# Kernel tuning notes

Hardware: AMD Instinct MI355X
Metric: run time of the kernel (lower is better)

The kernel has to match this reference:

```python
import jax, jax.numpy as jnp
import numpy as np

NUM_LEVELS = 16
FEATS_PER_LEVEL = 2
LOG2_HASHMAP = 19
TABLE_SIZE = 1 << LOG2_HASHMAP
BASE_RES = 16
DESIRED_RES = 4096
PER_LEVEL_SCALE = float(np.exp(np.log(DESIRED_RES / BASE_RES) / (NUM_LEVELS - 1)))
PRIMES = (np.uint32(1), np.uint32(2654435761), np.uint32(805459861))
N_POINTS = 2_000_000


def _level_features(x, table, level):
    # x: [N,3] in [0,1]; table: [TABLE_SIZE, F]
    scale = BASE_RES * (PER_LEVEL_SCALE ** level) - 1.0
    res = int(np.ceil(scale)) + 1
    dense = (res ** 3) <= TABLE_SIZE  # tcnn uses dense indexing when grid fits
    pos = x * scale + 0.5
    pos0 = jnp.floor(pos)
    w = pos - pos0                     # trilinear weights, [N,3]
    base = pos0.astype(jnp.uint32)
    out = jnp.zeros((x.shape[0], table.shape[1]), dtype=table.dtype)
    for c in range(8):                 # 8 corners of the voxel
        offs = [(c >> d) & 1 for d in range(3)]
        pc = [jnp.minimum(base[:, d] + np.uint32(offs[d]), np.uint32(res - 1)) for d in range(3)]
        if dense:
            idx = pc[0] + pc[1] * np.uint32(res) + pc[2] * np.uint32(res * res)
        else:
            idx = (pc[0] * PRIMES[0]) ^ (pc[1] * PRIMES[1]) ^ (pc[2] * PRIMES[2])
            idx = idx & np.uint32(TABLE_SIZE - 1)
        wt = jnp.ones(x.shape[0], dtype=x.dtype)
        for d in range(3):
            wt = wt * (w[:, d] if offs[d] else (1.0 - w[:, d]))
        out = out + wt[:, None] * table[idx.astype(jnp.int32)]
    return out


def hashgrid_encode(x, tables):
    # x: [N,3] in [0,1]; tables: [L, TABLE_SIZE, F] -> [N, L*F]
    return jnp.concatenate(
        [_level_features(x, tables[l], l) for l in range(NUM_LEVELS)], axis=-1)


def setup_inputs() -> dict:
    key = jax.random.key(0)
    k1, k2, k3, k4, k5 = jax.random.split(key, 5)
    points = jax.random.uniform(k1, (N_POINTS, 3), dtype=jnp.float32)
    # tcnn hashgrid init: uniform(-1e-4, 1e-4)
    tables = jax.random.uniform(k2, (NUM_LEVELS, TABLE_SIZE, FEATS_PER_LEVEL),
                                minval=-1e-4, maxval=1e-4, dtype=jnp.float32)
    def kaiming(k, fan_out, fan_in):
        bound = np.sqrt(2.0) * np.sqrt(3.0 / fan_in)
        return jax.random.uniform(k, (fan_out, fan_in), minval=-bound, maxval=bound,
                                  dtype=jnp.float32)
    W1 = kaiming(k3, 32, 32)
    W2 = kaiming(k4, 32, 32)
    W3 = kaiming(k5, 4, 32)
    aabb = jnp.stack([jnp.zeros(3, jnp.float32), jnp.ones(3, jnp.float32)])
    return {"points": points, "tables": tables, "W1": W1, "W2": W2, "W3": W3,
            "aabb": aabb}


def reference(points, tables, W1, W2, W3, aabb):
    texc = jnp.clip((points - aabb[0][None, :]) / (aabb[1] - aabb[0])[None, :], 0.0, 1.0)
    enc = hashgrid_encode(texc, tables)            # [N, 32]
    h = jax.nn.relu(enc @ W1.T)
    h = jax.nn.relu(h @ W2.T)
    out = h @ W3.T                                 # [N, 4]
    mn = jnp.array([0.0, 0.0, 0.0, 0.01], dtype=out.dtype)
    mx = jnp.array([1.0, 1.0, 1.0, 1.0], dtype=out.dtype)
    return jax.nn.sigmoid(out) * (mx - mn) + mn
```

## Files before the change

kernel.cpp:

```cpp
#include <hip/hip_runtime.h>
#include <cmath>


namespace {
constexpr int kLevels = 16;
constexpr unsigned kTableSize = 1u << 19;

typedef _Float16 half2_t __attribute__((ext_vector_type(2)));

struct LevelParams {
  float scale[kLevels];
  unsigned res[kLevels];
  int dense[kLevels];
};
}

__global__ __launch_bounds__(256)
void conv_tables_kernel(const float2* __restrict__ src, half2_t* __restrict__ dst,
                        int n_entries,
                        const float* __restrict__ W1, const float* __restrict__ W2,
                        const float* __restrict__ W3, half2_t* __restrict__ Wh)
{
  int i = blockIdx.x * blockDim.x + threadIdx.x;
  if (i < 512) {
    Wh[i] = half2_t{(_Float16)W1[2 * i], (_Float16)W1[2 * i + 1]};
  } else if (i < 1024) {
    int t = i - 512;
    Wh[512 + t] = half2_t{(_Float16)W2[2 * t], (_Float16)W2[2 * t + 1]};
  } else if (i < 1088) {
    int t = i - 1024;
    Wh[1024 + t] = half2_t{(_Float16)W3[2 * t], (_Float16)W3[2 * t + 1]};
  }
  int stride = gridDim.x * blockDim.x;
  for (; i < n_entries; i += stride) {
    float2 v = src[i];
    dst[i] = half2_t{(_Float16)v.x, (_Float16)v.y};
  }
}

__global__ __launch_bounds__(256)
void encode_kernel(const float* __restrict__ points,
                   const half2_t* __restrict__ tables,
                   const float* __restrict__ aabb,
                   half2_t* __restrict__ enc,
                   LevelParams lp, int n, int bpl)
{
  int l = blockIdx.x / bpl;
  int blk = blockIdx.x - l * bpl;
  int i0 = blk * 512 + threadIdx.x;
  int i1 = i0 + 256;
  if (i0 >= n) return;
  bool validB = (i1 < n);
  int i1c = validB ? i1 : i0;

  float a0x = aabb[0], a0y = aabb[1], a0z = aabb[2];
  float a1x = aabb[3], a1y = aabb[4], a1z = aabb[5];
  float s = lp.scale[l];
  unsigned res = lp.res[l];
  bool dense = (lp.dense[l] != 0);
  unsigned rm1 = res - 1u;
  unsigned res2 = res * res;
  const half2_t* tab = tables + (size_t)l * kTableSize;

  float xA = fminf(fmaxf((points[3 * i0 + 0] - a0x) / (a1x - a0x), 0.f), 1.f);
  float yA = fminf(fmaxf((points[3 * i0 + 1] - a0y) / (a1y - a0y), 0.f), 1.f);
  float zA = fminf(fmaxf((points[3 * i0 + 2] - a0z) / (a1z - a0z), 0.f), 1.f);
  float xB = fminf(fmaxf((points[3 * i1c + 0] - a0x) / (a1x - a0x), 0.f), 1.f);
  float yB = fminf(fmaxf((points[3 * i1c + 1] - a0y) / (a1y - a0y), 0.f), 1.f);
  float zB = fminf(fmaxf((points[3 * i1c + 2] - a0z) / (a1z - a0z), 0.f), 1.f);

  float fxA = xA * s + 0.5f, fyA = yA * s + 0.5f, fzA = zA * s + 0.5f;
  float fxB = xB * s + 0.5f, fyB = yB * s + 0.5f, fzB = zB * s + 0.5f;
  float fx0A = floorf(fxA), fy0A = floorf(fyA), fz0A = floorf(fzA);
  float fx0B = floorf(fxB), fy0B = floorf(fyB), fz0B = floorf(fzB);
  float wxA = fxA - fx0A, wyA = fyA - fy0A, wzA = fzA - fz0A;
  float wxB = fxB - fx0B, wyB = fyB - fy0B, wzB = fzB - fz0B;
  unsigned bxA = (unsigned)fx0A, byA = (unsigned)fy0A, bzA = (unsigned)fz0A;
  unsigned bxB = (unsigned)fx0B, byB = (unsigned)fy0B, bzB = (unsigned)fz0B;

  unsigned idxA[8], idxB[8];
  float wtA[8], wtB[8];
  #pragma unroll
  for (int c = 0; c < 8; ++c) {
    unsigned ox = (unsigned)(c & 1);
    unsigned oy = (unsigned)((c >> 1) & 1);
    unsigned oz = (unsigned)((c >> 2) & 1);
    unsigned pax = min(bxA + ox, rm1), pay = min(byA + oy, rm1), paz = min(bzA + oz, rm1);
    unsigned pbx = min(bxB + ox, rm1), pby = min(byB + oy, rm1), pbz = min(bzB + oz, rm1);
    if (dense) {
      idxA[c] = pax + pay * res + paz * res2;
      idxB[c] = pbx + pby * res + pbz * res2;
    } else {
      idxA[c] = (pax ^ (pay * 2654435761u) ^ (paz * 805459861u)) & (kTableSize - 1u);
      idxB[c] = (pbx ^ (pby * 2654435761u) ^ (pbz * 805459861u)) & (kTableSize - 1u);
    }
    wtA[c] = (ox ? wxA : 1.f - wxA) * (oy ? wyA : 1.f - wyA) * (oz ? wzA : 1.f - wzA);
    wtB[c] = (ox ? wxB : 1.f - wxB) * (oy ? wyB : 1.f - wyB) * (oz ? wzB : 1.f - wzB);
  }

  half2_t fA[8], fB[8];
  #pragma unroll
  for (int c = 0; c < 8; ++c) fA[c] = tab[idxA[c]];
  #pragma unroll
  for (int c = 0; c < 8; ++c) fB[c] = tab[idxB[c]];

  float a0 = 0.f, a1 = 0.f, b0 = 0.f, b1 = 0.f;
  #pragma unroll
  for (int c = 0; c < 8; ++c) {
    a0 += wtA[c] * (float)fA[c].x;
    a1 += wtA[c] * (float)fA[c].y;
    b0 += wtB[c] * (float)fB[c].x;
    b1 += wtB[c] * (float)fB[c].y;
  }
  enc[(size_t)l * n + i0] = half2_t{(_Float16)a0, (_Float16)a1};
  if (validB) enc[(size_t)l * n + i1] = half2_t{(_Float16)b0, (_Float16)b1};
}

__device__ __forceinline__ float dot2_acc(half2_t a, half2_t b, float c) {
#if __has_builtin(__builtin_amdgcn_fdot2)
  return __builtin_amdgcn_fdot2(a, b, c, false);
#else
  return c + (float)a.x * (float)b.x + (float)a.y * (float)b.y;
#endif
}

__global__ __launch_bounds__(256)
void mlp_kernel(const half2_t* __restrict__ enc,
                const half2_t* __restrict__ Wh,
                float* __restrict__ out, int n)
{
  int i = blockIdx.x * blockDim.x + threadIdx.x;
  if (i >= n) return;

  half2_t e[16];
  #pragma unroll
  for (int l = 0; l < kLevels; ++l) e[l] = enc[(size_t)l * n + i];

  const half2_t* W1h = Wh;
  const half2_t* W2h = Wh + 512;
  const half2_t* W3h = Wh + 1024;

  float h1f[32];
  #pragma unroll
  for (int j = 0; j < 32; ++j) {
    float acc = 0.f;
    #pragma unroll
    for (int k = 0; k < 16; ++k) acc = dot2_acc(e[k], W1h[16 * j + k], acc);
    h1f[j] = fmaxf(acc, 0.f);
  }
  half2_t h1[16];
  #pragma unroll
  for (int k = 0; k < 16; ++k)
    h1[k] = half2_t{(_Float16)h1f[2 * k], (_Float16)h1f[2 * k + 1]};

  float h2f[32];
  #pragma unroll
  for (int j = 0; j < 32; ++j) {
    float acc = 0.f;
    #pragma unroll
    for (int k = 0; k < 16; ++k) acc = dot2_acc(h1[k], W2h[16 * j + k], acc);
    h2f[j] = fmaxf(acc, 0.f);
  }
  half2_t h2[16];
  #pragma unroll
  for (int k = 0; k < 16; ++k)
    h2[k] = half2_t{(_Float16)h2f[2 * k], (_Float16)h2f[2 * k + 1]};

  float o[4];
  #pragma unroll
  for (int j = 0; j < 4; ++j) {
    float acc = 0.f;
    #pragma unroll
    for (int k = 0; k < 16; ++k) acc = dot2_acc(h2[k], W3h[16 * j + k], acc);
    o[j] = acc;
  }

  float4 r;
  r.x = 1.f / (1.f + __expf(-o[0]));
  r.y = 1.f / (1.f + __expf(-o[1]));
  r.z = 1.f / (1.f + __expf(-o[2]));
  r.w = 0.99f / (1.f + __expf(-o[3])) + 0.01f;
  reinterpret_cast<float4*>(out)[i] = r;
}

__global__ __launch_bounds__(256)
void hashgrid_mlp_kernel(const float* __restrict__ points,
                         const float* __restrict__ tables,
                         const float* __restrict__ W1,
                         const float* __restrict__ W2,
                         const float* __restrict__ W3,
                         const float* __restrict__ aabb,
                         float* __restrict__ out,
                         LevelParams lp, int n)
{
  int i = blockIdx.x * blockDim.x + threadIdx.x;
  if (i >= n) return;
  float a0x = aabb[0], a0y = aabb[1], a0z = aabb[2];
  float a1x = aabb[3], a1y = aabb[4], a1z = aabb[5];
  float x = fminf(fmaxf((points[3 * i + 0] - a0x) / (a1x - a0x), 0.f), 1.f);
  float y = fminf(fmaxf((points[3 * i + 1] - a0y) / (a1y - a0y), 0.f), 1.f);
  float z = fminf(fmaxf((points[3 * i + 2] - a0z) / (a1z - a0z), 0.f), 1.f);
  float enc[2 * kLevels];
  #pragma unroll
  for (int l = 0; l < kLevels; ++l) {
    float s = lp.scale[l];
    unsigned res = lp.res[l];
    bool dense = (lp.dense[l] != 0);
    unsigned rm1 = res - 1u;
    unsigned res2 = res * res;
    float fx = x * s + 0.5f, fy = y * s + 0.5f, fz = z * s + 0.5f;
    float fx0 = floorf(fx), fy0 = floorf(fy), fz0 = floorf(fz);
    float wx = fx - fx0, wy = fy - fy0, wz = fz - fz0;
    unsigned bx = (unsigned)fx0, by = (unsigned)fy0, bz = (unsigned)fz0;
    const float2* tab = reinterpret_cast<const float2*>(tables) + (size_t)l * kTableSize;
    float acc0 = 0.f, acc1 = 0.f;
    #pragma unroll
    for (int c = 0; c < 8; ++c) {
      unsigned ox = (unsigned)(c & 1);
      unsigned oy = (unsigned)((c >> 1) & 1);
      unsigned oz = (unsigned)((c >> 2) & 1);
      unsigned pcx = min(bx + ox, rm1);
      unsigned pcy = min(by + oy, rm1);
      unsigned pcz = min(bz + oz, rm1);
      unsigned idx;
      if (dense) idx = pcx + pcy * res + pcz * res2;
      else idx = (pcx ^ (pcy * 2654435761u) ^ (pcz * 805459861u)) & (kTableSize - 1u);
      float wt = (ox ? wx : 1.f - wx) * (oy ? wy : 1.f - wy) * (oz ? wz : 1.f - wz);
      float2 f = tab[idx];
      acc0 += wt * f.x;
      acc1 += wt * f.y;
    }
    enc[2 * l + 0] = acc0;
    enc[2 * l + 1] = acc1;
  }
  float h1[32];
  #pragma unroll
  for (int j = 0; j < 32; ++j) {
    float acc = 0.f;
    #pragma unroll
    for (int k = 0; k < 32; ++k) acc += enc[k] * W1[32 * j + k];
    h1[j] = fmaxf(acc, 0.f);
  }
  float h2[32];
  #pragma unroll
  for (int j = 0; j < 32; ++j) {
    float acc = 0.f;
    #pragma unroll
    for (int k = 0; k < 32; ++k) acc += h1[k] * W2[32 * j + k];
    h2[j] = fmaxf(acc, 0.f);
  }
  float o[4];
  #pragma unroll
  for (int j = 0; j < 4; ++j) {
    float acc = 0.f;
    #pragma unroll
    for (int k = 0; k < 32; ++k) acc += h2[k] * W3[32 * j + k];
    o[j] = acc;
  }
  float4 r;
  r.x = 1.f / (1.f + __expf(-o[0]));
  r.y = 1.f / (1.f + __expf(-o[1]));
  r.z = 1.f / (1.f + __expf(-o[2]));
  r.w = 0.99f / (1.f + __expf(-o[3])) + 0.01f;
  reinterpret_cast<float4*>(out)[i] = r;
}

extern "C" void kernel_launch(void* const* d_in, const int* in_sizes, int n_in,
                              void* d_out, int out_size, void* d_ws, size_t ws_size,
                              hipStream_t stream) {
  const float* points = (const float*)d_in[0];
  const float* tables = (const float*)d_in[1];
  const float* W1     = (const float*)d_in[2];
  const float* W2     = (const float*)d_in[3];
  const float* W3     = (const float*)d_in[4];
  const float* aabb   = (const float*)d_in[5];
  float* out = (float*)d_out;
  int n = in_sizes[0] / 3;

  LevelParams lp;
  const double pls = std::exp(std::log(4096.0 / 16.0) / 15.0);
  for (int l = 0; l < kLevels; ++l) {
    double s = 16.0 * std::pow(pls, (double)l) - 1.0;
    lp.scale[l] = (float)s;
    long long res = (long long)std::ceil(s) + 1;
    lp.res[l] = (unsigned)res;
    lp.dense[l] = (res * res * res <= (long long)kTableSize) ? 1 : 0;
  }

  const int block = 256;
  const size_t tab_f16_bytes = (size_t)kLevels * kTableSize * sizeof(half2_t);
  const size_t enc_bytes     = (size_t)kLevels * (size_t)n * sizeof(half2_t);
  const size_t w_bytes       = 1088 * sizeof(half2_t);
  const size_t needed = tab_f16_bytes + enc_bytes + w_bytes;

  if (ws_size >= needed) {
    half2_t* tab_f16 = reinterpret_cast<half2_t*>(d_ws);
    half2_t* enc = reinterpret_cast<half2_t*>((char*)d_ws + tab_f16_bytes);
    half2_t* Wh  = reinterpret_cast<half2_t*>((char*)d_ws + tab_f16_bytes + enc_bytes);

    const int n_entries = kLevels * (int)kTableSize;
    conv_tables_kernel<<<2048, block, 0, stream>>>(
        reinterpret_cast<const float2*>(tables), tab_f16, n_entries, W1, W2, W3, Wh);

    const int bpl = (n + 2 * block - 1) / (2 * block);
    encode_kernel<<<bpl * kLevels, block, 0, stream>>>(
        points, tab_f16, aabb, enc, lp, n, bpl);

    mlp_kernel<<<(n + block - 1) / block, block, 0, stream>>>(enc, Wh, out, n);
  } else {
    const int grid = (n + block - 1) / block;
    hashgrid_mlp_kernel<<<grid, block, 0, stream>>>(
        points, tables, W1, W2, W3, aabb, out, lp, n);
  }
}
```

Baseline: 909.2 us.

## Pair x-adjacent corner fetches into one 16-byte aligned table load

The encode kernel now processes one point per thread instead of two. For each of the four (y,z) corner pairs it issues a single aligned 16-byte load covering the x0 corner. When the x1 corner falls in the same 4-entry group (the dense case and often the hashed case, since x enters the hash by XOR), it is taken from that load. A separate 4-byte load is issued only when the two corners land in different groups. This cuts the number of scattered gather instructions, at the cost of wider loads, extra select logic and a change in per-thread parallelism.

After: 768.8 us. 15.4% less time.

```diff
diff --git a/kernel.cpp b/kernel.cpp
--- a/kernel.cpp
+++ b/kernel.cpp
@@ -5,8 +5,10 @@
 namespace {
 constexpr int kLevels = 16;
 constexpr unsigned kTableSize = 1u << 19;
+constexpr unsigned kMask = kTableSize - 1u;
 
 typedef _Float16 half2_t __attribute__((ext_vector_type(2)));
+typedef unsigned int u32;
 
 struct LevelParams {
   float scale[kLevels];
@@ -38,82 +40,89 @@
   }
 }
 
+__device__ __forceinline__ u32 sel4(uint4 v, u32 j) {
+  u32 lo = (j & 1u) ? v.y : v.x;
+  u32 hi = (j & 1u) ? v.w : v.z;
+  return (j & 2u) ? hi : lo;
+}
+
 __global__ __launch_bounds__(256)
 void encode_kernel(const float* __restrict__ points,
-                   const half2_t* __restrict__ tables,
+                   const u32* __restrict__ tables,
                    const float* __restrict__ aabb,
                    half2_t* __restrict__ enc,
                    LevelParams lp, int n, int bpl)
 {
   int l = blockIdx.x / bpl;
-  int blk = blockIdx.x - l * bpl;
-  int i0 = blk * 512 + threadIdx.x;
-  int i1 = i0 + 256;
-  if (i0 >= n) return;
-  bool validB = (i1 < n);
-  int i1c = validB ? i1 : i0;
+  int i = (blockIdx.x - l * bpl) * blockDim.x + threadIdx.x;
+  if (i >= n) return;
 
   float a0x = aabb[0], a0y = aabb[1], a0z = aabb[2];
   float a1x = aabb[3], a1y = aabb[4], a1z = aabb[5];
+  float x = fminf(fmaxf((points[3 * i + 0] - a0x) / (a1x - a0x), 0.f), 1.f);
+  float y = fminf(fmaxf((points[3 * i + 1] - a0y) / (a1y - a0y), 0.f), 1.f);
+  float z = fminf(fmaxf((points[3 * i + 2] - a0z) / (a1z - a0z), 0.f), 1.f);
+
   float s = lp.scale[l];
   unsigned res = lp.res[l];
   bool dense = (lp.dense[l] != 0);
   unsigned rm1 = res - 1u;
   unsigned res2 = res * res;
-  const half2_t* tab = tables + (size_t)l * kTableSize;
-
-  float xA = fminf(fmaxf((points[3 * i0 + 0] - a0x) / (a1x - a0x), 0.f), 1.f);
-  float yA = fminf(fmaxf((points[3 * i0 + 1] - a0y) / (a1y - a0y), 0.f), 1.f);
-  float zA = fminf(fmaxf((points[3 * i0 + 2] - a0z) / (a1z - a0z), 0.f), 1.f);
-  float xB = fminf(fmaxf((points[3 * i1c + 0] - a0x) / (a1x - a0x), 0.f), 1.f);
-  float yB = fminf(fmaxf((points[3 * i1c + 1] - a0y) / (a1y - a0y), 0.f), 1.f);
-  float zB = fminf(fmaxf((points[3 * i1c + 2] - a0z) / (a1z - a0z), 0.f), 1.f);
-
-  float fxA = xA * s + 0.5f, fyA = yA * s + 0.5f, fzA = zA * s + 0.5f;
-  float fxB = xB * s + 0.5f, fyB = yB * s + 0.5f, fzB = zB * s + 0.5f;
-  float fx0A = floorf(fxA), fy0A = floorf(fyA), fz0A = floorf(fzA);
-  float fx0B = floorf(fxB), fy0B = floorf(fyB), fz0B = floorf(fzB);
-  float wxA = fxA - fx0A, wyA = fyA - fy0A, wzA = fzA - fz0A;
-  float wxB = fxB - fx0B, wyB = fyB - fy0B, wzB = fzB - fz0B;
-  unsigned bxA = (unsigned)fx0A, byA = (unsigned)fy0A, bzA = (unsigned)fz0A;
-  unsigned bxB = (unsigned)fx0B, byB = (unsigned)fy0B, bzB = (unsigned)fz0B;
-
-  unsigned idxA[8], idxB[8];
-  float wtA[8], wtB[8];
-  #pragma unroll
-  for (int c = 0; c < 8; ++c) {
-    unsigned ox = (unsigned)(c & 1);
-    unsigned oy = (unsigned)((c >> 1) & 1);
-    unsigned oz = (unsigned)((c >> 2) & 1);
-    unsigned pax = min(bxA + ox, rm1), pay = min(byA + oy, rm1), paz = min(bzA + oz, rm1);
-    unsigned pbx = min(bxB + ox, rm1), pby = min(byB + oy, rm1), pbz = min(bzB + oz, rm1);
+  const u32* tab = tables + (size_t)l * kTableSize;
+
+  float fx = x * s + 0.5f, fy = y * s + 0.5f, fz = z * s + 0.5f;
+  float fx0 = floorf(fx), fy0 = floorf(fy), fz0 = floorf(fz);
+  float wx = fx - fx0, wy = fy - fy0, wz = fz - fz0;
+  unsigned bx = (unsigned)fx0, by = (unsigned)fy0, bz = (unsigned)fz0;
+
+  unsigned pcx0 = min(bx, rm1), pcx1 = min(bx + 1u, rm1);
+
+  u32 idx0[4], idx1[4];
+  #pragma unroll
+  for (int p = 0; p < 4; ++p) {
+    unsigned oy = (unsigned)(p & 1);
+    unsigned oz = (unsigned)(p >> 1);
+    unsigned pcy = min(by + oy, rm1);
+    unsigned pcz = min(bz + oz, rm1);
     if (dense) {
-      idxA[c] = pax + pay * res + paz * res2;
-      idxB[c] = pbx + pby * res + pbz * res2;
+      u32 b = pcy * res + pcz * res2;
+      idx0[p] = pcx0 + b;
+      idx1[p] = pcx1 + b;
     } else {
-      idxA[c] = (pax ^ (pay * 2654435761u) ^ (paz * 805459861u)) & (kTableSize - 1u);
-      idxB[c] = (pbx ^ (pby * 2654435761u) ^ (pbz * 805459861u)) & (kTableSize - 1u);
+      u32 h = (pcy * 2654435761u) ^ (pcz * 805459861u);
+      idx0[p] = (pcx0 ^ h) & kMask;
+      idx1[p] = (pcx1 ^ h) & kMask;
     }
-    wtA[c] = (ox ? wxA : 1.f - wxA) * (oy ? wyA : 1.f - wyA) * (oz ? wzA : 1.f - wzA);
-    wtB[c] = (ox ? wxB : 1.f - wxB) * (oy ? wyB : 1.f - wyB) * (oz ? wzB : 1.f - wzB);
-  }
-
-  half2_t fA[8], fB[8];
-  #pragma unroll
-  for (int c = 0; c < 8; ++c) fA[c] = tab[idxA[c]];
-  #pragma unroll
-  for (int c = 0; c < 8; ++c) fB[c] = tab[idxB[c]];
-
-  float a0 = 0.f, a1 = 0.f, b0 = 0.f, b1 = 0.f;
-  #pragma unroll
-  for (int c = 0; c < 8; ++c) {
-    a0 += wtA[c] * (float)fA[c].x;
-    a1 += wtA[c] * (float)fA[c].y;
-    b0 += wtB[c] * (float)fB[c].x;
-    b1 += wtB[c] * (float)fB[c].y;
-  }
-  enc[(size_t)l * n + i0] = half2_t{(_Float16)a0, (_Float16)a1};
-  if (validB) enc[(size_t)l * n + i1] = half2_t{(_Float16)b0, (_Float16)b1};
+  }
+
+  uint4 v[4];
+  #pragma unroll
+  for (int p = 0; p < 4; ++p)
+    v[p] = *reinterpret_cast<const uint4*>(tab + (idx0[p] & ~3u));
+
+  u32 e1x[4] = {0u, 0u, 0u, 0u};
+  #pragma unroll
+  for (int p = 0; p < 4; ++p) {
+    if ((idx0[p] ^ idx1[p]) >= 4u) e1x[p] = tab[idx1[p]];
+  }
+
+  float wx1 = wx, wx0 = 1.f - wx;
+  float acc0 = 0.f, acc1 = 0.f;
+  #pragma unroll
+  for (int p = 0; p < 4; ++p) {
+    unsigned oy = (unsigned)(p & 1);
+    unsigned oz = (unsigned)(p >> 1);
+    float wyz = (oy ? wy : 1.f - wy) * (oz ? wz : 1.f - wz);
+    u32 e0 = sel4(v[p], idx0[p] & 3u);
+    u32 e1g = sel4(v[p], idx1[p] & 3u);
+    u32 e1 = ((idx0[p] ^ idx1[p]) < 4u) ? e1g : e1x[p];
+    half2_t f0 = __builtin_bit_cast(half2_t, e0);
+    half2_t f1 = __builtin_bit_cast(half2_t, e1);
+    float w0 = wyz * wx0, w1 = wyz * wx1;
+    acc0 += w0 * (float)f0.x + w1 * (float)f1.x;
+    acc1 += w0 * (float)f0.y + w1 * (float)f1.y;
+  }
+  enc[(size_t)l * n + i] = half2_t{(_Float16)acc0, (_Float16)acc1};
 }
 
 __device__ __forceinline__ float dot2_acc(half2_t a, half2_t b, float c) {
@@ -224,7 +233,7 @@
       unsigned pcz = min(bz + oz, rm1);
       unsigned idx;
       if (dense) idx = pcx + pcy * res + pcz * res2;
-      else idx = (pcx ^ (pcy * 2654435761u) ^ (pcz * 805459861u)) & (kTableSize - 1u);
+      else idx = (pcx ^ (pcy * 2654435761u) ^ (pcz * 805459861u)) & kMask;
       float wt = (ox ? wx : 1.f - wx) * (oy ? wy : 1.f - wy) * (oz ? wz : 1.f - wz);
       float2 f = tab[idx];
       acc0 += wt * f.x;
@@ -302,9 +311,9 @@
     conv_tables_kernel<<<2048, block, 0, stream>>>(
         reinterpret_cast<const float2*>(tables), tab_f16, n_entries, W1, W2, W3, Wh);
 
-    const int bpl = (n + 2 * block - 1) / (2 * block);
+    const int bpl = (n + block - 1) / block;
     encode_kernel<<<bpl * kLevels, block, 0, stream>>>(
-        points, tab_f16, aabb, enc, lp, n, bpl);
+        points, reinterpret_cast<const u32*>(tab_f16), aabb, enc, lp, n, bpl);
 
     mlp_kernel<<<(n + block - 1) / block, block, 0, stream>>>(enc, Wh, out, n);
   } else {
```
